# Performance work log

Hardware: AMD Instinct MI355X
Metric: run time of the kernel (lower is better)

The kernel has to match this reference:

```python
import jax, jax.numpy as jnp
import numpy as np

N_NODES = 50000
N_EDGES = 600000
IN_C = 128
HID = 128
OUT_C = 32
N_GRAPHS = 64


def setup_inputs() -> dict:
    key = jax.random.key(0)
    ks = jax.random.split(key, 12)
    x = jax.random.normal(ks[0], (N_NODES, IN_C), dtype=jnp.float32)
    edge_index = jax.random.randint(ks[1], (2, N_EDGES), 0, N_NODES, dtype=jnp.int64)
    batch = jnp.sort(jax.random.randint(ks[2], (N_NODES,), 0, N_GRAPHS, dtype=jnp.int64))
    s1 = 1.0 / np.sqrt(IN_C)
    s2 = 1.0 / np.sqrt(HID)
    # SAGEConv: out = lin_l(mean_neighbors) + lin_r(x); lin_l has bias, lin_r has none
    W1l = jax.random.uniform(ks[3], (HID, IN_C), minval=-s1, maxval=s1, dtype=jnp.float32)
    b1 = jax.random.uniform(ks[4], (HID,), minval=-s1, maxval=s1, dtype=jnp.float32)
    W1r = jax.random.uniform(ks[5], (HID, IN_C), minval=-s1, maxval=s1, dtype=jnp.float32)
    W2l = jax.random.uniform(ks[6], (HID, HID), minval=-s2, maxval=s2, dtype=jnp.float32)
    b2 = jax.random.uniform(ks[7], (HID,), minval=-s2, maxval=s2, dtype=jnp.float32)
    W2r = jax.random.uniform(ks[8], (HID, HID), minval=-s2, maxval=s2, dtype=jnp.float32)
    Wlin = jax.random.uniform(ks[9], (OUT_C, HID), minval=-s2, maxval=s2, dtype=jnp.float32)
    blin = jax.random.uniform(ks[10], (OUT_C,), minval=-s2, maxval=s2, dtype=jnp.float32)
    return {"x": x, "edge_index": edge_index, "batch": batch,
            "W1l": W1l, "b1": b1, "W1r": W1r,
            "W2l": W2l, "b2": b2, "W2r": W2r,
            "Wlin": Wlin, "blin": blin}


def _sage_conv(x, src, dst, Wl, bl, Wr):
    # mean aggregation of source-node features onto destination nodes
    msg_sum = jax.ops.segment_sum(x[src], dst, num_segments=N_NODES)  # [N, d]
    deg = jax.ops.segment_sum(jnp.ones((src.shape[0],), x.dtype), dst, num_segments=N_NODES)
    mean = msg_sum / jnp.maximum(deg, 1.0)[:, None]
    return mean @ Wl.T + bl + x @ Wr.T


def reference(x, edge_index, batch, W1l, b1, W1r, W2l, b2, W2r, Wlin, blin):
    src, dst = edge_index[0], edge_index[1]
    h = jax.nn.relu(_sage_conv(x, src, dst, W1l, b1, W1r))
    h = jax.nn.relu(_sage_conv(h, src, dst, W2l, b2, W2r))
    # global mean pool over graph ids
    gsum = jax.ops.segment_sum(h, batch, num_segments=N_GRAPHS)        # [G, HID]
    cnt = jax.ops.segment_sum(jnp.ones((h.shape[0],), h.dtype), batch, num_segments=N_GRAPHS)
    pooled = gsum / jnp.maximum(cnt, 1.0)[:, None]
    return pooled @ Wlin.T + blin
```

## Files before the change

### kernel.cpp

```cpp
#include <hip/hip_runtime.h>
#include <hip/hip_fp16.h>

#define N_NODES 50000
#define N_EDGES 600000
#define N_GRAPHS 64
#define HID 128
#define OUT_C 32

#define N_SCAN_BLOCKS ((N_NODES + 255) / 256)
#define SCAN_FLAG 0x40000000

typedef __attribute__((ext_vector_type(8))) _Float16 half8;
typedef __attribute__((ext_vector_type(4))) float f32x4;

#define ZERO_INTS (2 * N_NODES + N_SCAN_BLOCKS)

__global__ __launch_bounds__(256) void prep_kernel(
    const float* __restrict__ x, const int* __restrict__ batch,
    const float* __restrict__ W1l, const float* __restrict__ W1r,
    const float* __restrict__ W2l, const float* __restrict__ W2r,
    __half* __restrict__ xh, __half* __restrict__ Wt1, __half* __restrict__ Wt2,
    int* __restrict__ zero_base, int* __restrict__ gstart) {
    const int b = blockIdx.x;
    const int t = threadIdx.x;
    const int gtid = b * 256 + t;
    const int gsz = gridDim.x * 256;
    for (int i = gtid; i < ZERO_INTS; i += gsz) zero_base[i] = 0;

    for (int i = gtid; i <= N_NODES; i += gsz) {
        if (i == 0) {
            int b1 = batch[0];
            for (int g = 0; g <= b1; ++g) gstart[g] = 0;
        } else if (i == N_NODES) {
            int b0 = batch[N_NODES - 1];
            for (int g = b0 + 1; g <= N_GRAPHS; ++g) gstart[g] = N_NODES;
        } else {
            int b0 = batch[i - 1], b1 = batch[i];
            for (int g = b0 + 1; g <= b1; ++g) gstart[g] = i;
        }
    }

    if (b < 16) {
        for (int i = gtid; i < 65536; i += 4096) {
            int which = i >> 15;
            int j = i & 32767;
            int n = j >> 8, k = j & 255;
            const float* Wl = which ? W2l : W1l;
            const float* Wr = which ? W2r : W1r;
            float a = (k < 128) ? Wl[n * 128 + k] : Wr[n * 128 + (k - 128)];
            (which ? Wt2 : Wt1)[j] = __float2half(a);
        }
    } else {
        int i = ((b - 16) * 256 + t) * 4;
        if (i < N_NODES * 128) {
            float4 v = *(const float4*)(x + i);
            __half2 a = __floats2half2_rn(v.x, v.y);
            __half2 c = __floats2half2_rn(v.z, v.w);
            uint2 st;
            st.x = *(const unsigned int*)&a;
            st.y = *(const unsigned int*)&c;
            *(uint2*)(xh + i) = st;
        }
    }
}

__global__ void deg_kernel(const int* __restrict__ dst, int* __restrict__ deg, int E) {
    int e = blockIdx.x * 256 + threadIdx.x;
    if (e < E) atomicAdd(&deg[dst[e]], 1);
}

__global__ __launch_bounds__(256) void scan_fused(
    const int* __restrict__ deg, int* __restrict__ bsum,
    int* __restrict__ rowptr, float* __restrict__ invdeg) {
    __shared__ int s[256];
    const int b = blockIdx.x;
    const int t = threadIdx.x;
    const int idx = b * 256 + t;
    const int v = (idx < N_NODES) ? deg[idx] : 0;
    s[t] = v;
    __syncthreads();
    for (int off = 1; off < 256; off <<= 1) {
        int u = (t >= off) ? s[t - off] : 0;
        __syncthreads();
        s[t] += u;
        __syncthreads();
    }
    const int incl = s[t];
    if (t == 255) atomicExch(&bsum[b], incl | SCAN_FLAG);

    int pv = 0;
    if (t < b) {
        int w;
        do { w = atomicAdd(&bsum[t], 0); } while (!(w & SCAN_FLAG));
        pv = w & ~SCAN_FLAG;
    }
    __syncthreads();
    s[t] = pv;
    __syncthreads();
    for (int off = 128; off > 0; off >>= 1) {
        if (t < off) s[t] += s[t + off];
        __syncthreads();
    }
    const int boffs = s[0];

    if (idx < N_NODES) {
        rowptr[idx] = boffs + incl - v;
        invdeg[idx] = 1.0f / fmaxf((float)v, 1.0f);
    }
    if (b == N_SCAN_BLOCKS - 1 && t == 255) rowptr[N_NODES] = boffs + incl;
}

__global__ void fill_kernel(const int* __restrict__ src, const int* __restrict__ dst,
                            const int* __restrict__ rowptr, int* __restrict__ cursor,
                            int* __restrict__ eidx, int E) {
    int e = blockIdx.x * 256 + threadIdx.x;
    if (e < E) {
        int d = dst[e];
        int pos = atomicAdd(&cursor[d], 1);
        eidx[rowptr[d] + pos] = src[e];
    }
}

#define AGG8(vv, aa, ab) { aa.x += (float)vv[0]; aa.y += (float)vv[1]; \
                           aa.z += (float)vv[2]; aa.w += (float)vv[3]; \
                           ab.x += (float)vv[4]; ab.y += (float)vv[5]; \
                           ab.z += (float)vv[6]; ab.w += (float)vv[7]; }

__global__ __launch_bounds__(256) void aggregate_f16(
    const __half* __restrict__ feat16, const int* __restrict__ rowptr,
    const int* __restrict__ eidx, const float* __restrict__ invdeg,
    __half* __restrict__ mean16) {
    const int wave = threadIdx.x >> 6;
    const int lane = threadIdx.x & 63;
    const int nh   = lane >> 4;
    const int sub  = lane & 15;
    const int node = blockIdx.x * 16 + wave * 4 + nh;
    const bool act = (node < N_NODES);
    int beg = 0, end = 0;
    if (act) { beg = rowptr[node]; end = rowptr[node + 1]; }
    const size_t coff = (size_t)sub * 8;

    float4 a0 = {0.f,0.f,0.f,0.f}, b0 = {0.f,0.f,0.f,0.f};
    float4 a1 = {0.f,0.f,0.f,0.f}, b1 = {0.f,0.f,0.f,0.f};
    float4 a2 = {0.f,0.f,0.f,0.f}, b2 = {0.f,0.f,0.f,0.f};
    float4 a3 = {0.f,0.f,0.f,0.f}, b3 = {0.f,0.f,0.f,0.f};
    int i = beg;
    for (; i + 8 <= end; i += 8) {
        int s0 = eidx[i+0], s1 = eidx[i+1], s2 = eidx[i+2], s3 = eidx[i+3];
        int s4 = eidx[i+4], s5 = eidx[i+5], s6 = eidx[i+6], s7 = eidx[i+7];
        half8 v0 = *(const half8*)(feat16 + (size_t)s0 * 128 + coff);
        half8 v1 = *(const half8*)(feat16 + (size_t)s1 * 128 + coff);
        half8 v2 = *(const half8*)(feat16 + (size_t)s2 * 128 + coff);
        half8 v3 = *(const half8*)(feat16 + (size_t)s3 * 128 + coff);
        half8 v4 = *(const half8*)(feat16 + (size_t)s4 * 128 + coff);
        half8 v5 = *(const half8*)(feat16 + (size_t)s5 * 128 + coff);
        half8 v6 = *(const half8*)(feat16 + (size_t)s6 * 128 + coff);
        half8 v7 = *(const half8*)(feat16 + (size_t)s7 * 128 + coff);
        AGG8(v0, a0, b0); AGG8(v1, a1, b1); AGG8(v2, a2, b2); AGG8(v3, a3, b3);
        AGG8(v4, a0, b0); AGG8(v5, a1, b1); AGG8(v6, a2, b2); AGG8(v7, a3, b3);
    }
    if (i + 4 <= end) {
        int s0 = eidx[i+0], s1 = eidx[i+1], s2 = eidx[i+2], s3 = eidx[i+3];
        half8 v0 = *(const half8*)(feat16 + (size_t)s0 * 128 + coff);
        half8 v1 = *(const half8*)(feat16 + (size_t)s1 * 128 + coff);
        half8 v2 = *(const half8*)(feat16 + (size_t)s2 * 128 + coff);
        half8 v3 = *(const half8*)(feat16 + (size_t)s3 * 128 + coff);
        AGG8(v0, a0, b0); AGG8(v1, a1, b1); AGG8(v2, a2, b2); AGG8(v3, a3, b3);
        i += 4;
    }
    if (i + 2 <= end) {
        int s0 = eidx[i+0], s1 = eidx[i+1];
        half8 v0 = *(const half8*)(feat16 + (size_t)s0 * 128 + coff);
        half8 v1 = *(const half8*)(feat16 + (size_t)s1 * 128 + coff);
        AGG8(v0, a0, b0); AGG8(v1, a1, b1);
        i += 2;
    }
    if (i < end) {
        int s0 = eidx[i];
        half8 v0 = *(const half8*)(feat16 + (size_t)s0 * 128 + coff);
        AGG8(v0, a0, b0);
    }

    if (act) {
        const float sc = invdeg[node];
        half8 r;
        r[0] = (_Float16)(((a0.x + a1.x) + (a2.x + a3.x)) * sc);
        r[1] = (_Float16)(((a0.y + a1.y) + (a2.y + a3.y)) * sc);
        r[2] = (_Float16)(((a0.z + a1.z) + (a2.z + a3.z)) * sc);
        r[3] = (_Float16)(((a0.w + a1.w) + (a2.w + a3.w)) * sc);
        r[4] = (_Float16)(((b0.x + b1.x) + (b2.x + b3.x)) * sc);
        r[5] = (_Float16)(((b0.y + b1.y) + (b2.y + b3.y)) * sc);
        r[6] = (_Float16)(((b0.z + b1.z) + (b2.z + b3.z)) * sc);
        r[7] = (_Float16)(((b0.w + b1.w) + (b2.w + b3.w)) * sc);
        *(half8*)(mean16 + (size_t)node * 128 + coff) = r;
    }
}

#define GBM 64
#define BPAD 8

__global__ __launch_bounds__(256) void sage_gemm_f16(
    const __half* __restrict__ mean16, const __half* __restrict__ feat16,
    const __half* __restrict__ Wt, const float* __restrict__ bias,
    __half* __restrict__ out16, int M) {
    __shared__ __align__(16) __half Bs[128][256 + BPAD];

    const int tid = threadIdx.x;
    const int wave = tid >> 6;
    const int lane = tid & 63;
    const int l15 = lane & 15;
    const int quad = lane >> 4;
    const int row0 = blockIdx.x * GBM;
    const int gi_a = min(row0 + wave * 16 + l15, M - 1);

    for (int id = tid; id < 128 * 32; id += 256) {
        int n = id >> 5;
        int kc = (id & 31) * 8;
        *(half8*)&Bs[n][kc] = *(const half8*)(Wt + (size_t)n * 256 + kc);
    }

    half8 af[8];
#pragma unroll
    for (int kb = 0; kb < 8; ++kb) {
        const int k0 = kb * 32;
        const __half* ap = (k0 < 128)
            ? (mean16 + (size_t)gi_a * 128 + k0 + quad * 8)
            : (feat16 + (size_t)gi_a * 128 + (k0 - 128) + quad * 8);
        af[kb] = *(const half8*)ap;
    }

    f32x4 acc[8];
#pragma unroll
    for (int t = 0; t < 8; ++t) acc[t] = (f32x4){0.f, 0.f, 0.f, 0.f};

    __syncthreads();

#pragma unroll
    for (int kb = 0; kb < 8; ++kb) {
#pragma unroll
        for (int t = 0; t < 8; ++t) {
            const half8 b = *(const half8*)&Bs[t * 16 + l15][kb * 32 + quad * 8];
            acc[t] = __builtin_amdgcn_mfma_f32_16x16x32_f16(af[kb], b, acc[t], 0, 0, 0);
        }
    }

#pragma unroll
    for (int r = 0; r < 4; ++r) {
        int gi = row0 + wave * 16 + quad * 4 + r;
        if (gi < M) {
#pragma unroll
            for (int t = 0; t < 8; ++t) {
                int col = t * 16 + l15;
                float v = fmaxf(acc[t][r] + bias[col], 0.f);
                out16[(size_t)gi * 128 + col] = __float2half(v);
            }
        }
    }
}

#define POOL_PARTS 4
__global__ __launch_bounds__(256) void pool_parts(
    const __half* __restrict__ h, const int* __restrict__ gstart,
    float* __restrict__ pooled_parts) {
    const int g = blockIdx.x >> 2;
    const int part = blockIdx.x & 3;
    const int start = gstart[g];
    const int end = gstart[g + 1];

    const int t = threadIdx.x;
    const int c4 = (t & 31) * 4;
    const int rg = t >> 5;
    float4 acc = {0.f, 0.f, 0.f, 0.f};
    for (int n = start + part * 8 + rg; n < end; n += 8 * POOL_PARTS) {
        const __half2* p = (const __half2*)(h + (size_t)n * 128 + c4);
        float2 f0 = __half22float2(p[0]);
        float2 f1 = __half22float2(p[1]);
        acc.x += f0.x; acc.y += f0.y; acc.z += f1.x; acc.w += f1.y;
    }
    __shared__ float sm[8][132];
    sm[rg][c4 + 0] = acc.x;
    sm[rg][c4 + 1] = acc.y;
    sm[rg][c4 + 2] = acc.z;
    sm[rg][c4 + 3] = acc.w;
    __syncthreads();
    if (t < 128) {
        float s = 0.f;
#pragma unroll
        for (int r = 0; r < 8; ++r) s += sm[r][t];
        pooled_parts[(size_t)blockIdx.x * 128 + t] = s;
    }
}

__global__ void final_kernel(const float* __restrict__ pooled_parts,
                             const int* __restrict__ gstart,
                             const float* __restrict__ Wlin, const float* __restrict__ blin,
                             float* __restrict__ out) {
    int g = blockIdx.x;
    int j = threadIdx.x;
    float inv = 1.0f / fmaxf((float)(gstart[g + 1] - gstart[g]), 1.0f);
    float sum = blin[j];
    const float* w = Wlin + j * 128;
    const float* p0 = pooled_parts + (size_t)(g * 4 + 0) * 128;
    const float* p1 = pooled_parts + (size_t)(g * 4 + 1) * 128;
    const float* p2 = pooled_parts + (size_t)(g * 4 + 2) * 128;
    const float* p3 = pooled_parts + (size_t)(g * 4 + 3) * 128;
    for (int c = 0; c < 128; ++c) {
        float p = (p0[c] + p1[c]) + (p2[c] + p3[c]);
        sum += p * inv * w[c];
    }
    out[g * 32 + j] = sum;
}

extern "C" void kernel_launch(void* const* d_in, const int* in_sizes, int n_in,
                              void* d_out, int out_size, void* d_ws, size_t ws_size,
                              hipStream_t stream) {
    const float* x    = (const float*)d_in[0];
    const int*   src  = (const int*)d_in[1];
    const int*   dst  = ((const int*)d_in[1]) + N_EDGES;
    const int*   batch= (const int*)d_in[2];
    const float* W1l  = (const float*)d_in[3];
    const float* b1   = (const float*)d_in[4];
    const float* W1r  = (const float*)d_in[5];
    const float* W2l  = (const float*)d_in[6];
    const float* b2   = (const float*)d_in[7];
    const float* W2r  = (const float*)d_in[8];
    const float* Wlin = (const float*)d_in[9];
    const float* blin = (const float*)d_in[10];
    float* out = (float*)d_out;

    __half* xh     = (__half*)d_ws;
    __half* mean16 = xh + 6400000;
    __half* h1_16  = mean16 + 6400000;
    __half* h2_16  = h1_16 + 6400000;
    __half* Wt1    = h2_16 + 6400000;
    __half* Wt2    = Wt1 + 32768;
    float* pooled_parts = (float*)(Wt2 + 32768);
    float* invdeg  = pooled_parts + 32768;
    int*   gstart  = (int*)(invdeg + N_NODES);
    int*   degi    = gstart + 65;
    int*   cursor  = degi + N_NODES;
    int*   bsum    = cursor + N_NODES;
    int*   rowptr  = bsum + N_SCAN_BLOCKS;
    int*   eidx    = rowptr + N_NODES + 1;

    prep_kernel<<<16 + (N_NODES * 128 / 4 + 255) / 256, 256, 0, stream>>>(
        x, batch, W1l, W1r, W2l, W2r, xh, Wt1, Wt2, degi, gstart);

    deg_kernel<<<(N_EDGES + 255) / 256, 256, 0, stream>>>(dst, degi, N_EDGES);
    scan_fused<<<N_SCAN_BLOCKS, 256, 0, stream>>>(degi, bsum, rowptr, invdeg);
    fill_kernel<<<(N_EDGES + 255) / 256, 256, 0, stream>>>(src, dst, rowptr, cursor, eidx, N_EDGES);

    const int gemm_grid = (N_NODES + GBM - 1) / GBM;
    const int agg_grid = (N_NODES + 15) / 16;

    aggregate_f16<<<agg_grid, 256, 0, stream>>>(xh, rowptr, eidx, invdeg, mean16);
    sage_gemm_f16<<<gemm_grid, 256, 0, stream>>>(mean16, xh, Wt1, b1, h1_16, N_NODES);

    aggregate_f16<<<agg_grid, 256, 0, stream>>>(h1_16, rowptr, eidx, invdeg, mean16);
    sage_gemm_f16<<<gemm_grid, 256, 0, stream>>>(mean16, h1_16, Wt2, b2, h2_16, N_NODES);

    pool_parts<<<N_GRAPHS * POOL_PARTS, 256, 0, stream>>>(h2_16, gstart, pooled_parts);
    final_kernel<<<N_GRAPHS, 32, 0, stream>>>(pooled_parts, gstart, Wlin, blin, out);
}
```

Measured before the change: 259.2 us.

## Regroup preprocessing kernels and batch edge-index prefetch in aggregation

Preprocessing is split into a small zeroing kernel, a combined degree-count, graph-start and weight-cast kernel, and a combined CSR fill and x-to-half cast kernel. The x cast now runs alongside the fill instead of ahead of the degree pass. The aggregation kernel prefetches the first 32 edge indices with one coalesced load per lane and broadcasts them by shuffle. It then gathers 16 neighbours per iteration, masking the tail with a weight instead of separate remainder branches. This shortens serial index loads and adds memory-level parallelism, at the cost of wasted gathers for low-degree nodes and more register pressure.

```diff
diff --git a/kernel.cpp b/kernel.cpp
--- a/kernel.cpp
+++ b/kernel.cpp
@@ -15,33 +15,42 @@
 
 #define ZERO_INTS (2 * N_NODES + N_SCAN_BLOCKS)
 
-__global__ __launch_bounds__(256) void prep_kernel(
-    const float* __restrict__ x, const int* __restrict__ batch,
+__global__ __launch_bounds__(256) void zero_kernel(int* __restrict__ zb) {
+    int i = blockIdx.x * 256 + threadIdx.x;
+    if (i < ZERO_INTS) zb[i] = 0;
+}
+
+#define DEG_BLOCKS ((N_EDGES + 255) / 256)
+#define GST_BLOCKS ((N_NODES + 256) / 256)
+
+__global__ __launch_bounds__(256) void deg_gst_w(
+    const int* __restrict__ dst, int* __restrict__ degi,
+    const int* __restrict__ batch, int* __restrict__ gstart,
     const float* __restrict__ W1l, const float* __restrict__ W1r,
     const float* __restrict__ W2l, const float* __restrict__ W2r,
-    __half* __restrict__ xh, __half* __restrict__ Wt1, __half* __restrict__ Wt2,
-    int* __restrict__ zero_base, int* __restrict__ gstart) {
+    __half* __restrict__ Wt1, __half* __restrict__ Wt2) {
     const int b = blockIdx.x;
     const int t = threadIdx.x;
-    const int gtid = b * 256 + t;
-    const int gsz = gridDim.x * 256;
-    for (int i = gtid; i < ZERO_INTS; i += gsz) zero_base[i] = 0;
-
-    for (int i = gtid; i <= N_NODES; i += gsz) {
-        if (i == 0) {
-            int b1 = batch[0];
-            for (int g = 0; g <= b1; ++g) gstart[g] = 0;
-        } else if (i == N_NODES) {
-            int b0 = batch[N_NODES - 1];
-            for (int g = b0 + 1; g <= N_GRAPHS; ++g) gstart[g] = N_NODES;
-        } else {
-            int b0 = batch[i - 1], b1 = batch[i];
-            for (int g = b0 + 1; g <= b1; ++g) gstart[g] = i;
-        }
-    }
-
-    if (b < 16) {
-        for (int i = gtid; i < 65536; i += 4096) {
+    if (b < DEG_BLOCKS) {
+        int e = b * 256 + t;
+        if (e < N_EDGES) atomicAdd(&degi[dst[e]], 1);
+    } else if (b < DEG_BLOCKS + GST_BLOCKS) {
+        int i = (b - DEG_BLOCKS) * 256 + t;
+        if (i <= N_NODES) {
+            if (i == 0) {
+                int b1 = batch[0];
+                for (int g = 0; g <= b1; ++g) gstart[g] = 0;
+            } else if (i == N_NODES) {
+                int b0 = batch[N_NODES - 1];
+                for (int g = b0 + 1; g <= N_GRAPHS; ++g) gstart[g] = N_NODES;
+            } else {
+                int b0 = batch[i - 1], b1 = batch[i];
+                for (int g = b0 + 1; g <= b1; ++g) gstart[g] = i;
+            }
+        }
+    } else {
+        int local = (b - DEG_BLOCKS - GST_BLOCKS) * 256 + t;
+        for (int i = local; i < 65536; i += 4096) {
             int which = i >> 15;
             int j = i & 32767;
             int n = j >> 8, k = j & 255;
@@ -50,23 +59,7 @@
             float a = (k < 128) ? Wl[n * 128 + k] : Wr[n * 128 + (k - 128)];
             (which ? Wt2 : Wt1)[j] = __float2half(a);
         }
-    } else {
-        int i = ((b - 16) * 256 + t) * 4;
-        if (i < N_NODES * 128) {
-            float4 v = *(const float4*)(x + i);
-            __half2 a = __floats2half2_rn(v.x, v.y);
-            __half2 c = __floats2half2_rn(v.z, v.w);
-            uint2 st;
-            st.x = *(const unsigned int*)&a;
-            st.y = *(const unsigned int*)&c;
-            *(uint2*)(xh + i) = st;
-        }
-    }
-}
-
-__global__ void deg_kernel(const int* __restrict__ dst, int* __restrict__ deg, int E) {
-    int e = blockIdx.x * 256 + threadIdx.x;
-    if (e < E) atomicAdd(&deg[dst[e]], 1);
+    }
 }
 
 __global__ __launch_bounds__(256) void scan_fused(
@@ -110,88 +103,102 @@
     if (b == N_SCAN_BLOCKS - 1 && t == 255) rowptr[N_NODES] = boffs + incl;
 }
 
-__global__ void fill_kernel(const int* __restrict__ src, const int* __restrict__ dst,
-                            const int* __restrict__ rowptr, int* __restrict__ cursor,
-                            int* __restrict__ eidx, int E) {
-    int e = blockIdx.x * 256 + threadIdx.x;
-    if (e < E) {
-        int d = dst[e];
-        int pos = atomicAdd(&cursor[d], 1);
-        eidx[rowptr[d] + pos] = src[e];
-    }
-}
-
-#define AGG8(vv, aa, ab) { aa.x += (float)vv[0]; aa.y += (float)vv[1]; \
-                           aa.z += (float)vv[2]; aa.w += (float)vv[3]; \
-                           ab.x += (float)vv[4]; ab.y += (float)vv[5]; \
-                           ab.z += (float)vv[6]; ab.w += (float)vv[7]; }
+__global__ __launch_bounds__(256) void fill_cast(
+    const int* __restrict__ src, const int* __restrict__ dst,
+    const int* __restrict__ rowptr, int* __restrict__ cursor,
+    int* __restrict__ eidx,
+    const float* __restrict__ x, __half* __restrict__ xh) {
+    const int b = blockIdx.x;
+    const int t = threadIdx.x;
+    if (b < DEG_BLOCKS) {
+        int e = b * 256 + t;
+        if (e < N_EDGES) {
+            int d = dst[e];
+            int pos = atomicAdd(&cursor[d], 1);
+            eidx[rowptr[d] + pos] = src[e];
+        }
+    } else {
+        int i = ((b - DEG_BLOCKS) * 256 + t) * 4;
+        if (i < N_NODES * 128) {
+            float4 v = *(const float4*)(x + i);
+            __half2 a = __floats2half2_rn(v.x, v.y);
+            __half2 c = __floats2half2_rn(v.z, v.w);
+            uint2 st;
+            st.x = *(const unsigned int*)&a;
+            st.y = *(const unsigned int*)&c;
+            *(uint2*)(xh + i) = st;
+        }
+    }
+}
 
 __global__ __launch_bounds__(256) void aggregate_f16(
     const __half* __restrict__ feat16, const int* __restrict__ rowptr,
     const int* __restrict__ eidx, const float* __restrict__ invdeg,
     __half* __restrict__ mean16) {
-    const int wave = threadIdx.x >> 6;
-    const int lane = threadIdx.x & 63;
-    const int nh   = lane >> 4;
+    const int tid  = threadIdx.x;
+    const int lane = tid & 63;
     const int sub  = lane & 15;
-    const int node = blockIdx.x * 16 + wave * 4 + nh;
+    const int gbase = lane & 48;
+    const int node = blockIdx.x * 16 + (tid >> 4);
     const bool act = (node < N_NODES);
     int beg = 0, end = 0;
     if (act) { beg = rowptr[node]; end = rowptr[node + 1]; }
+    const int deg = end - beg;
     const size_t coff = (size_t)sub * 8;
 
-    float4 a0 = {0.f,0.f,0.f,0.f}, b0 = {0.f,0.f,0.f,0.f};
-    float4 a1 = {0.f,0.f,0.f,0.f}, b1 = {0.f,0.f,0.f,0.f};
-    float4 a2 = {0.f,0.f,0.f,0.f}, b2 = {0.f,0.f,0.f,0.f};
-    float4 a3 = {0.f,0.f,0.f,0.f}, b3 = {0.f,0.f,0.f,0.f};
-    int i = beg;
-    for (; i + 8 <= end; i += 8) {
-        int s0 = eidx[i+0], s1 = eidx[i+1], s2 = eidx[i+2], s3 = eidx[i+3];
-        int s4 = eidx[i+4], s5 = eidx[i+5], s6 = eidx[i+6], s7 = eidx[i+7];
-        half8 v0 = *(const half8*)(feat16 + (size_t)s0 * 128 + coff);
-        half8 v1 = *(const half8*)(feat16 + (size_t)s1 * 128 + coff);
-        half8 v2 = *(const half8*)(feat16 + (size_t)s2 * 128 + coff);
-        half8 v3 = *(const half8*)(feat16 + (size_t)s3 * 128 + coff);
-        half8 v4 = *(const half8*)(feat16 + (size_t)s4 * 128 + coff);
-        half8 v5 = *(const half8*)(feat16 + (size_t)s5 * 128 + coff);
-        half8 v6 = *(const half8*)(feat16 + (size_t)s6 * 128 + coff);
-        half8 v7 = *(const half8*)(feat16 + (size_t)s7 * 128 + coff);
-        AGG8(v0, a0, b0); AGG8(v1, a1, b1); AGG8(v2, a2, b2); AGG8(v3, a3, b3);
-        AGG8(v4, a0, b0); AGG8(v5, a1, b1); AGG8(v6, a2, b2); AGG8(v7, a3, b3);
-    }
-    if (i + 4 <= end) {
-        int s0 = eidx[i+0], s1 = eidx[i+1], s2 = eidx[i+2], s3 = eidx[i+3];
-        half8 v0 = *(const half8*)(feat16 + (size_t)s0 * 128 + coff);
-        half8 v1 = *(const half8*)(feat16 + (size_t)s1 * 128 + coff);
-        half8 v2 = *(const half8*)(feat16 + (size_t)s2 * 128 + coff);
-        half8 v3 = *(const half8*)(feat16 + (size_t)s3 * 128 + coff);
-        AGG8(v0, a0, b0); AGG8(v1, a1, b1); AGG8(v2, a2, b2); AGG8(v3, a3, b3);
-        i += 4;
-    }
-    if (i + 2 <= end) {
-        int s0 = eidx[i+0], s1 = eidx[i+1];
-        half8 v0 = *(const half8*)(feat16 + (size_t)s0 * 128 + coff);
-        half8 v1 = *(const half8*)(feat16 + (size_t)s1 * 128 + coff);
-        AGG8(v0, a0, b0); AGG8(v1, a1, b1);
-        i += 2;
-    }
-    if (i < end) {
-        int s0 = eidx[i];
-        half8 v0 = *(const half8*)(feat16 + (size_t)s0 * 128 + coff);
-        AGG8(v0, a0, b0);
+    int pre0 = 0, pre1 = 0;
+    if (deg > 0) {
+        pre0 = eidx[min(beg + sub,      end - 1)];
+        pre1 = eidx[min(beg + 16 + sub, end - 1)];
+    }
+
+    float4 a[4], bb[4];
+#pragma unroll
+    for (int g = 0; g < 4; ++g) { a[g] = (float4){0.f,0.f,0.f,0.f}; bb[g] = (float4){0.f,0.f,0.f,0.f}; }
+
+    for (int j0 = 0; j0 < deg; j0 += 16) {
+        int idx[16];
+        if (j0 == 0) {
+#pragma unroll
+            for (int k = 0; k < 16; ++k) idx[k] = __shfl(pre0, gbase + k);
+        } else if (j0 == 16) {
+#pragma unroll
+            for (int k = 0; k < 16; ++k) idx[k] = __shfl(pre1, gbase + k);
+        } else {
+#pragma unroll
+            for (int k = 0; k < 16; ++k) idx[k] = eidx[min(beg + j0 + k, end - 1)];
+        }
+        half8 v[16];
+#pragma unroll
+        for (int k = 0; k < 16; ++k)
+            v[k] = *(const half8*)(feat16 + (size_t)idx[k] * 128 + coff);
+        const int rem = deg - j0;
+#pragma unroll
+        for (int k = 0; k < 16; ++k) {
+            const float w = (k < rem) ? 1.0f : 0.0f;
+            const int g = k & 3;
+            a[g].x  += w * (float)v[k][0];
+            a[g].y  += w * (float)v[k][1];
+            a[g].z  += w * (float)v[k][2];
+            a[g].w  += w * (float)v[k][3];
+            bb[g].x += w * (float)v[k][4];
+            bb[g].y += w * (float)v[k][5];
+            bb[g].z += w * (float)v[k][6];
+            bb[g].w += w * (float)v[k][7];
+        }
     }
 
     if (act) {
         const float sc = invdeg[node];
         half8 r;
-        r[0] = (_Float16)(((a0.x + a1.x) + (a2.x + a3.x)) * sc);
-        r[1] = (_Float16)(((a0.y + a1.y) + (a2.y + a3.y)) * sc);
-        r[2] = (_Float16)(((a0.z + a1.z) + (a2.z + a3.z)) * sc);
-        r[3] = (_Float16)(((a0.w + a1.w) + (a2.w + a3.w)) * sc);
-        r[4] = (_Float16)(((b0.x + b1.x) + (b2.x + b3.x)) * sc);
-        r[5] = (_Float16)(((b0.y + b1.y) + (b2.y + b3.y)) * sc);
-        r[6] = (_Float16)(((b0.z + b1.z) + (b2.z + b3.z)) * sc);
-        r[7] = (_Float16)(((b0.w + b1.w) + (b2.w + b3.w)) * sc);
+        r[0] = (_Float16)(((a[0].x + a[1].x) + (a[2].x + a[3].x)) * sc);
+        r[1] = (_Float16)(((a[0].y + a[1].y) + (a[2].y + a[3].y)) * sc);
+        r[2] = (_Float16)(((a[0].z + a[1].z) + (a[2].z + a[3].z)) * sc);
+        r[3] = (_Float16)(((a[0].w + a[1].w) + (a[2].w + a[3].w)) * sc);
+        r[4] = (_Float16)(((bb[0].x + bb[1].x) + (bb[2].x + bb[3].x)) * sc);
+        r[5] = (_Float16)(((bb[0].y + bb[1].y) + (bb[2].y + bb[3].y)) * sc);
+        r[6] = (_Float16)(((bb[0].z + bb[1].z) + (bb[2].z + bb[3].z)) * sc);
+        r[7] = (_Float16)(((bb[0].w + bb[1].w) + (bb[2].w + bb[3].w)) * sc);
         *(half8*)(mean16 + (size_t)node * 128 + coff) = r;
     }
 }
@@ -343,12 +350,15 @@
     int*   rowptr  = bsum + N_SCAN_BLOCKS;
     int*   eidx    = rowptr + N_NODES + 1;
 
-    prep_kernel<<<16 + (N_NODES * 128 / 4 + 255) / 256, 256, 0, stream>>>(
-        x, batch, W1l, W1r, W2l, W2r, xh, Wt1, Wt2, degi, gstart);
-
-    deg_kernel<<<(N_EDGES + 255) / 256, 256, 0, stream>>>(dst, degi, N_EDGES);
+    zero_kernel<<<(ZERO_INTS + 255) / 256, 256, 0, stream>>>(degi);
+
+    deg_gst_w<<<DEG_BLOCKS + GST_BLOCKS + 16, 256, 0, stream>>>(
+        dst, degi, batch, gstart, W1l, W1r, W2l, W2r, Wt1, Wt2);
+
     scan_fused<<<N_SCAN_BLOCKS, 256, 0, stream>>>(degi, bsum, rowptr, invdeg);
-    fill_kernel<<<(N_EDGES + 255) / 256, 256, 0, stream>>>(src, dst, rowptr, cursor, eidx, N_EDGES);
+
+    fill_cast<<<DEG_BLOCKS + (N_NODES * 128 / 4 + 255) / 256, 256, 0, stream>>>(
+        src, dst, rowptr, cursor, eidx, x, xh);
 
     const int gemm_grid = (N_NODES + GBM - 1) / GBM;
     const int agg_grid = (N_NODES + 15) / 16;
```

New measurement: 252.0 us. -2.8%, faster.
